# Kernel tuning notes

Hardware: AMD Instinct MI355X
Metric: run time of the kernel (lower is better)

## Reference

```python
import jax, jax.numpy as jnp
import numpy as np

H = 8        # n_heads (== n_kv_heads)
D = 128      # head_dim
WINDOW = 16  # sliding window (left); causal => right window = 0
EPS = 1e-6   # qk_norm_eps


def rms_norm(x, w, eps=EPS):
    # RMSNorm over last dim with learnable scale
    ms = jnp.mean(jnp.square(x), axis=-1, keepdims=True)
    return x * jax.lax.rsqrt(ms + eps) * w


def setup_inputs() -> dict:
    key = jax.random.key(0)
    ks = jax.random.split(key, 5)
    B, S, dim = 4, 2048, 1024
    scale = 1.0 / np.sqrt(dim)
    return {
        "x": jax.random.normal(ks[0], (B, S, dim), jnp.float32),
        "wq": jax.random.normal(ks[1], (dim, dim), jnp.float32) * scale,
        "wk": jax.random.normal(ks[2], (dim, dim), jnp.float32) * scale,
        "wv": jax.random.normal(ks[3], (dim, dim), jnp.float32) * scale,
        "wo": jax.random.normal(ks[4], (dim, dim), jnp.float32) * scale,
        "q_norm_w": jnp.ones((dim,), jnp.float32),
        "k_norm_w": jnp.ones((dim,), jnp.float32),
    }


def reference(x, wq, wk, wv, wo, q_norm_w, k_norm_w):
    B, S, dim = x.shape
    # projections (torch Linear: x @ W.T)
    xq = rms_norm(x @ wq.T, q_norm_w)
    xk = rms_norm(x @ wk.T, k_norm_w)
    xv = x @ wv.T
    q = xq.reshape(B, S, H, D)
    k = xk.reshape(B, S, H, D)
    v = xv.reshape(B, S, H, D)

    # ALiBi slopes for 8 heads (power of two): 2^-1 .. 2^-8
    slopes = jnp.exp2(-jnp.arange(1, H + 1, dtype=jnp.float32))
    pos = jnp.arange(S)
    rel = pos[None, :] - pos[:, None]          # [S, S], rel[i, j] = j - i
    bias = slopes[:, None, None] * rel.astype(x.dtype)   # [H, S, S]
    masked = (rel > 0) | (rel < -WINDOW)       # causal + sliding window
    bias = jnp.where(masked[None], -jnp.inf, bias)

    scores = jnp.einsum('bqhd,bkhd->bhqk', q, k) / np.sqrt(D) + bias[None]
    attn = jax.nn.softmax(scores, axis=-1)
    out = jnp.einsum('bhqk,bkhd->bqhd', attn, v).reshape(B, S, H * D)
    return out @ wo.T
```

## Files before the change

kernel.cpp:

```cpp
#include <hip/hip_runtime.h>
#include <math.h>

#define NHEADS 8
#define HDIM   128
#define WIN    16
#define DIM    1024
#define QKVDIM 3072
#define SEQ    2048
#define BATCH  4
#define MROWS  (BATCH * SEQ)
#define RMS_EPS 1e-6f
#define PLANE  ((size_t)MROWS * HDIM)

typedef __bf16 bf16x8 __attribute__((ext_vector_type(8)));
typedef unsigned short u16x8 __attribute__((ext_vector_type(8)));
typedef float  f32x4  __attribute__((ext_vector_type(4)));

__device__ __forceinline__ unsigned short f2b(float f) {
    union { float f; unsigned u; } c; c.f = f;
    return (unsigned short)((c.u + 0x7FFFu + ((c.u >> 16) & 1u)) >> 16);
}
__device__ __forceinline__ float b2f(unsigned short u) {
    union { unsigned u; float f; } c; c.u = ((unsigned)u) << 16; return c.f;
}
__device__ __forceinline__ bf16x8 u2b(u16x8 u) {
    union { u16x8 u; bf16x8 b; } c; c.u = u; return c.b;
}

__global__ __launch_bounds__(256) void cast_all(const float* __restrict__ x,
                                                const float* __restrict__ w0,
                                                const float* __restrict__ w1,
                                                const float* __restrict__ w2,
                                                const float* __restrict__ w3,
                                                unsigned short* __restrict__ xb,
                                                unsigned short* __restrict__ wb,
                                                float* __restrict__ sumsq)
{
    const int b = blockIdx.x;
    const int t = threadIdx.x;
    if (b >= 12288) {
        ((float4*)sumsq)[(b - 12288) * 256 + t] = make_float4(0.f, 0.f, 0.f, 0.f);
        return;
    }
    const float* src;
    unsigned short* dst;
    int i;
    if (b < 8192) {
        i = b * 256 + t;
        src = x; dst = xb;
    } else {
        const int bb = b - 8192;
        const int which = bb >> 10;
        i = (bb & 1023) * 256 + t;
        src = which == 0 ? w0 : which == 1 ? w1 : which == 2 ? w2 : w3;
        dst = wb + (size_t)which * DIM * DIM;
    }
    const float4 v = ((const float4*)src)[i];
    ushort4 o;
    o.x = f2b(v.x); o.y = f2b(v.y); o.z = f2b(v.z); o.w = f2b(v.w);
    ((ushort4*)dst)[i] = o;
}

#define BARR do { asm volatile("s_barrier" ::: "memory"); __builtin_amdgcn_sched_barrier(0); } while (0)
#define WAITV(N) asm volatile("s_waitcnt vmcnt(" #N ")" ::: "memory")

#define LDA8(b) { \
    _Pragma("unroll") for (int il = 0; il < 4; ++il) { \
        const int rr = (wm * 64 + il * 16 + frow) * 64; \
        af[il][0] = *(const bf16x8*)&As[b][rr + cs0]; \
        af[il][1] = *(const bf16x8*)&As[b][rr + cs1]; \
    } }

#define LDB4(bh, b, bgr) { \
    _Pragma("unroll") for (int jl = 0; jl < 2; ++jl) { \
        const int rr = (wn * 64 + (bh) * 32 + jl * 16 + frow) * 64; \
        bgr[jl][0] = *(const bf16x8*)&Bs[b][rr + cs0]; \
        bgr[jl][1] = *(const bf16x8*)&Bs[b][rr + cs1]; \
    } }

#define MMA16(bh, bgr) { \
    __builtin_amdgcn_s_setprio(1); \
    _Pragma("unroll") for (int il = 0; il < 4; ++il) \
    _Pragma("unroll") for (int jl = 0; jl < 2; ++jl) { \
        acc[il][(bh)*2+jl] = __builtin_amdgcn_mfma_f32_16x16x32_bf16(af[il][0], bgr[jl][0], acc[il][(bh)*2+jl], 0, 0, 0); \
        acc[il][(bh)*2+jl] = __builtin_amdgcn_mfma_f32_16x16x32_bf16(af[il][1], bgr[jl][1], acc[il][(bh)*2+jl], 0, 0, 0); \
    } \
    __builtin_amdgcn_s_setprio(0); }

#define STAGE_A(b, kt) { \
    _Pragma("unroll") for (int s2 = 0; s2 < 4; ++s2) { \
        const int rb = s2 * 64; \
        __builtin_amdgcn_global_load_lds( \
            (const __attribute__((address_space(1))) void*)(gA + (size_t)rb * K + (kt)), \
            (__attribute__((address_space(3))) void*)&As[b][(rb + wid * 8) * 64], 16, 0, 0); \
    } }

#define STAGE_B(b, kt) { \
    _Pragma("unroll") for (int s2 = 0; s2 < 2; ++s2) { \
        const int rb = s2 * 64; \
        __builtin_amdgcn_global_load_lds( \
            (const __attribute__((address_space(1))) void*)(gB + (size_t)rb * K + (kt)), \
            (__attribute__((address_space(3))) void*)&Bs[b][(rb + wid * 8) * 64], 16, 0, 0); \
    } }

template <typename TC, bool PLANAR>
__global__ __launch_bounds__(512, 2) void gemm_nt_bm256(const unsigned short* __restrict__ A,
                                                        const unsigned short* __restrict__ B,
                                                        TC* __restrict__ C,
                                                        float* __restrict__ sumsq,
                                                        int M, int N, int K)
{
    __shared__ __align__(16) __bf16 As[2][256 * 64];
    __shared__ __align__(16) __bf16 Bs[2][128 * 64];

    const int t    = threadIdx.x;
    const int wid  = t >> 6;
    const int lane = t & 63;
    const int wm   = wid >> 1;
    const int wn   = wid & 1;
    const int bm0  = blockIdx.y * 256;
    const int bn0  = blockIdx.x * 128;

    const int frow = lane & 15;
    const int quad = lane >> 4;
    const int cs0  = ((quad    ) ^ (frow & 7)) * 8;
    const int cs1  = ((quad + 4) ^ (frow & 7)) * 8;

    const int lr = lane >> 3;
    const int lc = (lane & 7) ^ lr;
    const unsigned short* gA = A + (size_t)(bm0 + wid * 8 + lr) * K + lc * 8;
    const unsigned short* gB = B + (size_t)(bn0 + wid * 8 + lr) * K + lc * 8;

    f32x4 acc[4][4];
    #pragma unroll
    for (int i = 0; i < 4; ++i)
        #pragma unroll
        for (int j = 0; j < 4; ++j)
            #pragma unroll
            for (int e = 0; e < 4; ++e) acc[i][j][e] = 0.f;

    bf16x8 af[4][2], bg0[2][2], bg1[2][2];

    const int NI = K >> 6;

    STAGE_B(0, 0); STAGE_A(0, 0); STAGE_B(1, 64);
    WAITV(2);
    BARR;

    for (int i = 0; i < NI; ++i) {
        const int cur = i & 1;
        const int nxt = cur ^ 1;
        const int kt  = i << 6;
        LDA8(cur); LDB4(0, cur, bg0); LDB4(1, cur, bg1);
        if (i + 1 < NI) STAGE_A(nxt, kt + 64);
        BARR; MMA16(0, bg0); BARR;
        if (i + 2 < NI) STAGE_B(cur, kt + 128);
        BARR; MMA16(1, bg1);
        if (i + 2 < NI)      { WAITV(2); }
        else if (i + 1 < NI) { WAITV(0); }
        BARR;
    }

    const int m_base = bm0 + wm * 64;
    const int n_base = bn0 + wn * 64;
    if constexpr (PLANAR) {
        size_t cb[4];
        #pragma unroll
        for (int j = 0; j < 4; ++j) {
            const int nb = n_base + j * 16;
            cb[j] = (size_t)(nb >> 7) * PLANE + (nb & 127);
        }
        #pragma unroll
        for (int il = 0; il < 4; ++il)
            #pragma unroll
            for (int r = 0; r < 4; ++r) {
                const size_t row = m_base + il * 16 + quad * 4 + r;
                #pragma unroll
                for (int j = 0; j < 4; ++j)
                    ((unsigned short*)C)[cb[j] + row * HDIM + frow] = f2b(acc[il][j][r]);
            }
        if (sumsq != nullptr && bn0 < 2 * DIM) {
            const int which = bn0 >> 10;
            #pragma unroll
            for (int il = 0; il < 4; ++il)
                #pragma unroll
                for (int r = 0; r < 4; ++r) {
                    float p = acc[il][0][r] * acc[il][0][r] + acc[il][1][r] * acc[il][1][r]
                            + acc[il][2][r] * acc[il][2][r] + acc[il][3][r] * acc[il][3][r];
                    p += __shfl_xor(p, 1, 64);
                    p += __shfl_xor(p, 2, 64);
                    p += __shfl_xor(p, 4, 64);
                    p += __shfl_xor(p, 8, 64);
                    if (frow == 0)
                        atomicAdd(&sumsq[(size_t)(m_base + il * 16 + quad * 4 + r) * 2 + which], p);
                }
        }
    } else {
        #pragma unroll
        for (int il = 0; il < 4; ++il)
            #pragma unroll
            for (int r = 0; r < 4; ++r) {
                TC* crow = C + (size_t)(m_base + il * 16 + quad * 4 + r) * N + n_base + frow;
                #pragma unroll
                for (int j = 0; j < 4; ++j)
                    crow[j * 16] = acc[il][j][r];
            }
    }
}

__global__ __launch_bounds__(256) void attn_mfma(const unsigned short* __restrict__ qkvp,
                                                 const float* __restrict__ sumsq,
                                                 const float* __restrict__ qw,
                                                 const float* __restrict__ kw,
                                                 unsigned short* __restrict__ o)
{
    __shared__ __align__(16) unsigned short Klds[80 * 136];
    __shared__ __align__(16) unsigned short Vt[128 * 88];
    __shared__ __align__(16) unsigned short Plds[4 * 16 * 40];

    const int t  = threadIdx.x;
    const int qb = blockIdx.x;
    const int h  = blockIdx.y;
    const int r0 = qb * 64;
    const int i0 = r0 & (SEQ - 1);
    const int bb = r0 - i0;

    const unsigned short* qg = qkvp + (size_t)h * PLANE;
    const unsigned short* kg = qkvp + (size_t)(NHEADS + h) * PLANE;
    const unsigned short* vg = qkvp + (size_t)(2 * NHEADS + h) * PLANE;

    #pragma unroll
    for (int it = 0; it < 5; ++it) {
        const int c = it * 256 + t;
        {
            const int lr2 = c >> 4, c8 = c & 15;
            const int ks = i0 - 16 + lr2;
            const int rc = ks < 0 ? 0 : ks;
            const u16x8 kv = *(const u16x8*)(kg + (size_t)(bb + rc) * HDIM + c8 * 8);
            *(u16x8*)&Klds[lr2 * 136 + c8 * 8] = kv;
        }
        {
            const int c8 = c / 80, lr2 = c - c8 * 80;
            const int ks = i0 - 16 + lr2;
            const int rc = ks < 0 ? 0 : ks;
            const u16x8 vv = *(const u16x8*)(vg + (size_t)(bb + rc) * HDIM + c8 * 8);
            #pragma unroll
            for (int e = 0; e < 8; ++e)
                Vt[(c8 * 8 + e) * 88 + lr2] = vv[e];
        }
    }
    __syncthreads();

    const int w    = t >> 6;
    const int lane = t & 63;
    const int frow = lane & 15;
    const int quad = lane >> 4;
    const int fk   = quad * 8;

    const size_t qrow = (size_t)(r0 + w * 16 + frow) * HDIM;
    const int kidx0   = i0 - 16 + w * 16 + frow;
    const int kr0     = kidx0 < 0 ? 0 : kidx0;

    f32x4 s0 = {0.f, 0.f, 0.f, 0.f}, s1 = {0.f, 0.f, 0.f, 0.f};
    #pragma unroll
    for (int kt = 0; kt < 4; ++kt) {
        const u16x8 qa = *(const u16x8*)(qg + qrow + kt * 32 + fk);
        u16x8 qn;
        #pragma unroll
        for (int e = 0; e < 8; ++e) {
            const int d = h * HDIM + kt * 32 + fk + e;
            qn[e] = f2b(b2f(qa[e]) * qw[d] * kw[d]);
        }
        const bf16x8 af = u2b(qn);
        const bf16x8 b0 = *(const bf16x8*)&Klds[(w * 16 + frow) * 136 + kt * 32 + fk];
        const bf16x8 b1 = *(const bf16x8*)&Klds[(w * 16 + 16 + frow) * 136 + kt * 32 + fk];
        s0 = __builtin_amdgcn_mfma_f32_16x16x32_bf16(af, b0, s0, 0, 0, 0);
        s1 = __builtin_amdgcn_mfma_f32_16x16x32_bf16(af, b1, s1, 0, 0, 0);
    }

    const float ksc0 = rsqrtf(sumsq[(size_t)(bb + kr0) * 2 + 1] * (1.0f / DIM) + RMS_EPS);
    const float ksc1 = rsqrtf(sumsq[(size_t)(r0 + w * 16 + frow) * 2 + 1] * (1.0f / DIM) + RMS_EPS);
    float qs[4];
    #pragma unroll
    for (int r = 0; r < 4; ++r)
        qs[r] = rsqrtf(sumsq[(size_t)(r0 + w * 16 + quad * 4 + r) * 2] * (1.0f / DIM) + RMS_EPS);

    const float scl   = 0.088388347648318447f;
    const float slope = exp2f(-(float)(h + 1));
    const bool  lead  = (i0 == 0) && (w == 0);
    const int   col   = frow;
    float inv[4];
    #pragma unroll
    for (int r = 0; r < 4; ++r) {
        const int m = quad * 4 + r;
        const float sc0 = scl * qs[r] * ksc0;
        const float sc1 = scl * qs[r] * ksc1;
        float v0 = (col < m || lead) ? -1e30f : s0[r] * sc0 + slope * (float)(col - 16 - m);
        float v1 = (col > m)         ? -1e30f : s1[r] * sc1 + slope * (float)(col - m);
        float mx = fmaxf(v0, v1);
        #pragma unroll
        for (int off = 1; off < 16; off <<= 1) mx = fmaxf(mx, __shfl_xor(mx, off, 64));
        const float e0 = __expf(v0 - mx);
        const float e1 = __expf(v1 - mx);
        float sm = e0 + e1;
        #pragma unroll
        for (int off = 1; off < 16; off <<= 1) sm += __shfl_xor(sm, off, 64);
        inv[r] = 1.0f / sm;
        Plds[(w * 16 + m) * 40 + col]      = f2b(e0);
        Plds[(w * 16 + m) * 40 + 16 + col] = f2b(e1);
    }

    const bf16x8 pf = *(const bf16x8*)&Plds[(w * 16 + frow) * 40 + fk];
    f32x4 oa[8];
    #pragma unroll
    for (int nt = 0; nt < 8; ++nt) {
        oa[nt][0] = 0.f; oa[nt][1] = 0.f; oa[nt][2] = 0.f; oa[nt][3] = 0.f;
        const bf16x8 vf = *(const bf16x8*)&Vt[(nt * 16 + frow) * 88 + w * 16 + fk];
        oa[nt] = __builtin_amdgcn_mfma_f32_16x16x32_bf16(pf, vf, oa[nt], 0, 0, 0);
    }

    #pragma unroll
    for (int nt = 0; nt < 8; ++nt)
        #pragma unroll
        for (int r = 0; r < 4; ++r) {
            const int m = quad * 4 + r;
            o[(size_t)(r0 + w * 16 + m) * DIM + h * HDIM + nt * 16 + col] =
                f2b(oa[nt][r] * inv[r]);
        }
}

extern "C" void kernel_launch(void* const* d_in, const int* in_sizes, int n_in,
                              void* d_out, int out_size, void* d_ws, size_t ws_size,
                              hipStream_t stream)
{
    const float* x  = (const float*)d_in[0];
    const float* wq = (const float*)d_in[1];
    const float* wk = (const float*)d_in[2];
    const float* wv = (const float*)d_in[3];
    const float* wo = (const float*)d_in[4];
    const float* qw = (const float*)d_in[5];
    const float* kw = (const float*)d_in[6];
    float* out = (float*)d_out;

    unsigned short* xb   = (unsigned short*)d_ws;
    unsigned short* wb   = xb + (size_t)MROWS * DIM;
    unsigned short* qkvp = wb + (size_t)4 * DIM * DIM;
    unsigned short* ob   = qkvp + (size_t)MROWS * QKVDIM;
    float*          ssq  = (float*)(ob + (size_t)MROWS * DIM);
    unsigned short* wob  = wb + (size_t)3 * DIM * DIM;

    cast_all<<<12304, 256, 0, stream>>>(x, wq, wk, wv, wo, xb, wb, ssq);

    gemm_nt_bm256<unsigned short, true><<<dim3(QKVDIM / 128, MROWS / 256), 512, 0, stream>>>(
        xb, wb, qkvp, ssq, MROWS, QKVDIM, DIM);

    attn_mfma<<<dim3(MROWS / 64, NHEADS), 256, 0, stream>>>(qkvp, ssq, qw, kw, ob);

    gemm_nt_bm256<float, false><<<dim3(DIM / 128, MROWS / 256), 512, 0, stream>>>(
        ob, wob, out, nullptr, MROWS, DIM, DIM);
}
```

Baseline: 212.6 us.

## Add 256x256-tile GEMM for Q/K projections and split V projection launch

Adds a new 256x256-tile bf16 MFMA GEMM with a double-buffered, interleaved LDS staging schedule. It computes the Q and K projections along with their RMS sum-of-squares, while V is computed by the existing 256x128 kernel in a separate launch. The larger tile is meant to raise arithmetic intensity and cut global and LDS traffic per FLOP. In exchange it needs double the LDS, holds a larger accumulator, adds an extra launch, and the sumsq code is removed from the old kernel.

```diff
diff --git a/kernel.cpp b/kernel.cpp
--- a/kernel.cpp
+++ b/kernel.cpp
@@ -64,6 +64,156 @@
 #define BARR do { asm volatile("s_barrier" ::: "memory"); __builtin_amdgcn_sched_barrier(0); } while (0)
 #define WAITV(N) asm volatile("s_waitcnt vmcnt(" #N ")" ::: "memory")
 
+#define QLDA8(mh, b) { \
+    _Pragma("unroll") for (int il = 0; il < 4; ++il) { \
+        const int rr = (wm2 * 128 + (mh) * 64 + il * 16 + frow) * 64; \
+        af[il][0] = *(const bf16x8*)&As[b][rr + cs0]; \
+        af[il][1] = *(const bf16x8*)&As[b][rr + cs1]; \
+    } }
+
+#define QLDB4(nh, b, bgr) { \
+    _Pragma("unroll") for (int jl = 0; jl < 2; ++jl) { \
+        const int rr = (wn4 * 64 + (nh) * 32 + jl * 16 + frow) * 64; \
+        bgr[jl][0] = *(const bf16x8*)&Bs[b][rr + cs0]; \
+        bgr[jl][1] = *(const bf16x8*)&Bs[b][rr + cs1]; \
+    } }
+
+#define QMMA16(mh, nh, bgr) { \
+    __builtin_amdgcn_s_setprio(1); \
+    _Pragma("unroll") for (int il = 0; il < 4; ++il) \
+    _Pragma("unroll") for (int jl = 0; jl < 2; ++jl) { \
+        acc[(mh)*4+il][(nh)*2+jl] = __builtin_amdgcn_mfma_f32_16x16x32_bf16(af[il][0], bgr[jl][0], acc[(mh)*4+il][(nh)*2+jl], 0, 0, 0); \
+        acc[(mh)*4+il][(nh)*2+jl] = __builtin_amdgcn_mfma_f32_16x16x32_bf16(af[il][1], bgr[jl][1], acc[(mh)*4+il][(nh)*2+jl], 0, 0, 0); \
+    } \
+    __builtin_amdgcn_s_setprio(0); }
+
+#define QSTAGE_A(b, half, kt) { \
+    _Pragma("unroll") for (int s2 = 0; s2 < 2; ++s2) { \
+        const int rb = (half) * 128 + s2 * 64; \
+        __builtin_amdgcn_global_load_lds( \
+            (const __attribute__((address_space(1))) void*)(gA + (size_t)rb * K + (kt)), \
+            (__attribute__((address_space(3))) void*)&As[b][(rb + wid * 8) * 64], 16, 0, 0); \
+    } }
+
+#define QSTAGE_B(b, half, kt) { \
+    _Pragma("unroll") for (int s2 = 0; s2 < 2; ++s2) { \
+        const int rb = (half) * 128 + s2 * 64; \
+        __builtin_amdgcn_global_load_lds( \
+            (const __attribute__((address_space(1))) void*)(gB + (size_t)rb * K + (kt)), \
+            (__attribute__((address_space(3))) void*)&Bs[b][(rb + wid * 8) * 64], 16, 0, 0); \
+    } }
+
+__global__ __launch_bounds__(512, 2) void gemm_nt_256(const unsigned short* __restrict__ A,
+                                                      const unsigned short* __restrict__ B,
+                                                      unsigned short* __restrict__ Cq,
+                                                      float* __restrict__ sumsq,
+                                                      int M, int N, int K)
+{
+    __shared__ __align__(16) __bf16 As[2][256 * 64];
+    __shared__ __align__(16) __bf16 Bs[2][256 * 64];
+
+    const int t    = threadIdx.x;
+    const int wid  = t >> 6;
+    const int lane = t & 63;
+    const int wm2  = wid >> 2;
+    const int wn4  = wid & 3;
+    const int bm0  = blockIdx.y * 256;
+    const int bn0  = blockIdx.x * 256;
+
+    const int frow = lane & 15;
+    const int quad = lane >> 4;
+    const int cs0  = ((quad    ) ^ (frow & 7)) * 8;
+    const int cs1  = ((quad + 4) ^ (frow & 7)) * 8;
+
+    const int lr = lane >> 3;
+    const int lc = (lane & 7) ^ lr;
+    const unsigned short* gA = A + (size_t)(bm0 + wid * 8 + lr) * K + lc * 8;
+    const unsigned short* gB = B + (size_t)(bn0 + wid * 8 + lr) * K + lc * 8;
+
+    f32x4 acc[8][4];
+    #pragma unroll
+    for (int i = 0; i < 8; ++i)
+        #pragma unroll
+        for (int j = 0; j < 4; ++j)
+            #pragma unroll
+            for (int e = 0; e < 4; ++e) acc[i][j][e] = 0.f;
+
+    bf16x8 af[4][2], bg0[2][2], bg1[2][2];
+
+    const int NI = K >> 7;
+
+    QSTAGE_B(0, 0, 0); QSTAGE_B(0, 1, 0); QSTAGE_A(0, 0, 0); QSTAGE_A(0, 1, 0);
+    QSTAGE_B(1, 0, 64); QSTAGE_B(1, 1, 64);
+    WAITV(4);
+    BARR;
+
+    for (int i = 0; i < NI; ++i) {
+        const bool last = (i == NI - 1);
+        const int kt0 = i << 7;
+        QLDA8(0, 0); QLDB4(0, 0, bg0);
+        QSTAGE_A(1, 0, kt0 + 64);
+        BARR; QMMA16(0, 0, bg0); BARR;
+        QLDB4(1, 0, bg1);
+        QSTAGE_A(1, 1, kt0 + 64);
+        BARR; QMMA16(0, 1, bg1); BARR;
+        QLDA8(1, 0);
+        if (!last) QSTAGE_B(0, 0, kt0 + 128);
+        BARR; QMMA16(1, 1, bg1); BARR;
+        if (!last) QSTAGE_B(0, 1, kt0 + 128);
+        BARR; QMMA16(1, 0, bg0);
+        if (last) { WAITV(0); } else { WAITV(4); }
+        BARR;
+        QLDA8(0, 1); QLDB4(0, 1, bg0);
+        if (!last) QSTAGE_A(0, 0, kt0 + 128);
+        BARR; QMMA16(0, 0, bg0); BARR;
+        QLDB4(1, 1, bg1);
+        if (!last) QSTAGE_A(0, 1, kt0 + 128);
+        BARR; QMMA16(0, 1, bg1); BARR;
+        QLDA8(1, 1);
+        if (!last) QSTAGE_B(1, 0, kt0 + 192);
+        BARR; QMMA16(1, 1, bg1); BARR;
+        if (!last) QSTAGE_B(1, 1, kt0 + 192);
+        BARR; QMMA16(1, 0, bg0);
+        if (!last) { WAITV(4); }
+        BARR;
+    }
+
+    const int m_base = bm0 + wm2 * 128;
+    const int n_base = bn0 + wn4 * 64;
+    size_t cb[4];
+    #pragma unroll
+    for (int j = 0; j < 4; ++j) {
+        const int nb = n_base + j * 16;
+        cb[j] = (size_t)(nb >> 7) * PLANE + (nb & 127);
+    }
+    #pragma unroll
+    for (int i2 = 0; i2 < 8; ++i2)
+        #pragma unroll
+        for (int r = 0; r < 4; ++r) {
+            const size_t row = m_base + i2 * 16 + quad * 4 + r;
+            #pragma unroll
+            for (int j = 0; j < 4; ++j)
+                Cq[cb[j] + row * HDIM + frow] = f2b(acc[i2][j][r]);
+        }
+
+    if (sumsq != nullptr && bn0 < 2 * DIM) {
+        const int which = bn0 >> 10;
+        #pragma unroll
+        for (int i2 = 0; i2 < 8; ++i2)
+            #pragma unroll
+            for (int r = 0; r < 4; ++r) {
+                float p = acc[i2][0][r] * acc[i2][0][r] + acc[i2][1][r] * acc[i2][1][r]
+                        + acc[i2][2][r] * acc[i2][2][r] + acc[i2][3][r] * acc[i2][3][r];
+                p += __shfl_xor(p, 1, 64);
+                p += __shfl_xor(p, 2, 64);
+                p += __shfl_xor(p, 4, 64);
+                p += __shfl_xor(p, 8, 64);
+                if (frow == 0)
+                    atomicAdd(&sumsq[(size_t)(m_base + i2 * 16 + quad * 4 + r) * 2 + which], p);
+            }
+    }
+}
+
 #define LDA8(b) { \
     _Pragma("unroll") for (int il = 0; il < 4; ++il) { \
         const int rr = (wm * 64 + il * 16 + frow) * 64; \
@@ -179,22 +329,6 @@
                 for (int j = 0; j < 4; ++j)
                     ((unsigned short*)C)[cb[j] + row * HDIM + frow] = f2b(acc[il][j][r]);
             }
-        if (sumsq != nullptr && bn0 < 2 * DIM) {
-            const int which = bn0 >> 10;
-            #pragma unroll
-            for (int il = 0; il < 4; ++il)
-                #pragma unroll
-                for (int r = 0; r < 4; ++r) {
-                    float p = acc[il][0][r] * acc[il][0][r] + acc[il][1][r] * acc[il][1][r]
-                            + acc[il][2][r] * acc[il][2][r] + acc[il][3][r] * acc[il][3][r];
-                    p += __shfl_xor(p, 1, 64);
-                    p += __shfl_xor(p, 2, 64);
-                    p += __shfl_xor(p, 4, 64);
-                    p += __shfl_xor(p, 8, 64);
-                    if (frow == 0)
-                        atomicAdd(&sumsq[(size_t)(m_base + il * 16 + quad * 4 + r) * 2 + which], p);
-                }
-        }
     } else {
         #pragma unroll
         for (int il = 0; il < 4; ++il)
@@ -347,12 +481,16 @@
     unsigned short* qkvp = wb + (size_t)4 * DIM * DIM;
     unsigned short* ob   = qkvp + (size_t)MROWS * QKVDIM;
     float*          ssq  = (float*)(ob + (size_t)MROWS * DIM);
+    unsigned short* wvb  = wb + (size_t)2 * DIM * DIM;
     unsigned short* wob  = wb + (size_t)3 * DIM * DIM;
 
     cast_all<<<12304, 256, 0, stream>>>(x, wq, wk, wv, wo, xb, wb, ssq);
 
-    gemm_nt_bm256<unsigned short, true><<<dim3(QKVDIM / 128, MROWS / 256), 512, 0, stream>>>(
-        xb, wb, qkvp, ssq, MROWS, QKVDIM, DIM);
+    gemm_nt_256<<<dim3(2048 / 256, MROWS / 256), 512, 0, stream>>>(
+        xb, wb, qkvp, ssq, MROWS, 2048, DIM);
+
+    gemm_nt_bm256<unsigned short, true><<<dim3(1024 / 128, MROWS / 256), 512, 0, stream>>>(
+        xb, wvb, qkvp + (size_t)16 * PLANE, nullptr, MROWS, 1024, DIM);
 
     attn_mfma<<<dim3(MROWS / 64, NHEADS), 256, 0, stream>>>(qkvp, ssq, qw, kw, ob);
 
```

New measurement: 222.3 us. 1.05x slower.
